# Optimization experiments

Measured on AMD Instinct MI355X. Metric: run time of the kernel, lower is better.

Reference implementation:

```python
import jax, jax.numpy as jnp
import numpy as np

B, S, E = 4, 4096, 512

def setup_inputs() -> dict:
    key = jax.random.key(0)
    ks = jax.random.split(key, 9)
    scale = 1.0 / np.sqrt(E)  # keep linear weights at realistic init scale
    return {
        "query": jax.random.normal(ks[0], (B, S, E), jnp.float32),
        "key":   jax.random.normal(ks[1], (B, S, E), jnp.float32),
        "value": jax.random.normal(ks[2], (B, S, E), jnp.float32),
        "Wq": jax.random.normal(ks[3], (E, E), jnp.float32) * scale,
        "bq": jax.random.normal(ks[4], (E,), jnp.float32) * scale,
        "Wk": jax.random.normal(ks[5], (E, E), jnp.float32) * scale,
        "bk": jax.random.normal(ks[6], (E,), jnp.float32) * scale,
        "Wv": jax.random.normal(ks[7], (E, E), jnp.float32) * scale,
        "bv": jax.random.normal(ks[8], (E,), jnp.float32) * scale,
    }

def reference(query, key, value, Wq, bq, Wk, bk, Wv, bv):
    # torch Linear: x @ W^T + b
    q = jnp.einsum('bse,oe->bso', query, Wq) + bq
    k = jnp.einsum('bse,oe->bso', key,   Wk) + bk
    v = jnp.einsum('bse,oe->bso', value, Wv) + bv
    # NOTE: module applies NO 1/sqrt(d) scaling (faithful to source)
    scores = jnp.einsum('bqd,bkd->bqk', q, k)          # [B,S,S] materialized
    attn = jax.nn.softmax(scores, axis=-1)
    # dropout is identity in eval / for deterministic reference
    return jnp.einsum('bqk,bkd->bqd', attn, v)         # [B,S,E]
```

## Files before the change

kernel.cpp:

```cpp
#include <hip/hip_runtime.h>

typedef __attribute__((ext_vector_type(8))) _Float16 f16x8;
typedef __attribute__((ext_vector_type(4))) _Float16 f16x4;
typedef __attribute__((ext_vector_type(4))) float f32x4;

#define NB 4
#define NS 4096
#define NE 512

__device__ __forceinline__ f16x8 cvt2(float4 a, float4 b) {
    f16x8 r;
    r[0] = (_Float16)a.x; r[1] = (_Float16)a.y; r[2] = (_Float16)a.z; r[3] = (_Float16)a.w;
    r[4] = (_Float16)b.x; r[5] = (_Float16)b.y; r[6] = (_Float16)b.z; r[7] = (_Float16)b.w;
    return r;
}
__device__ __forceinline__ void gload_lds16(const void* g, void* l) {
    __builtin_amdgcn_global_load_lds(
        (const __attribute__((address_space(1))) void*)g,
        (__attribute__((address_space(3))) void*)l, 16, 0, 0);
}

__global__ __launch_bounds__(256) void proj_kernel(
    const float* __restrict__ Xq, const float* __restrict__ Xk,
    const float* __restrict__ Xv,
    const float* __restrict__ Wq, const float* __restrict__ Wk,
    const float* __restrict__ Wv,
    const float* __restrict__ bq, const float* __restrict__ bk,
    const float* __restrict__ bv,
    _Float16* __restrict__ oq, _Float16* __restrict__ ok,
    _Float16* __restrict__ ovt, int b0)
{
    __shared__ __align__(16) _Float16 As[128 * 32];
    __shared__ __align__(16) _Float16 Bs[128 * 32];
    const int t = threadIdx.x;
    const int w = t >> 6, ln = t & 63;
    const int which = blockIdx.y;
    const float* X    = (which == 0) ? Xq : ((which == 1) ? Xk : Xv);
    const float* W    = (which == 0) ? Wq : ((which == 1) ? Wk : Wv);
    const float* bias = (which == 0) ? bq : ((which == 1) ? bk : bv);

    const int m0 = (blockIdx.x >> 2) * 128;
    const int n0 = (blockIdx.x & 3) * 128;

    const int srow  = t >> 1;
    const int shalf = (t & 1) * 16;
    const float* gA = X + ((size_t)b0 * NS + m0 + srow) * NE + shalf;
    const float* gB = W + (size_t)(n0 + srow) * NE + shalf;
    _Float16* lA = &As[srow * 32 + shalf];
    _Float16* lB = &Bs[srow * 32 + shalf];

    f32x4 acc[4][4] = {};
    const int wm = (w >> 1) * 64, wn = (w & 1) * 64;
    const int lcol = ln & 15, lq = ln >> 4;

    for (int k0 = 0; k0 < NE; k0 += 32) {
        float4 xa0 = *(const float4*)(gA + k0);
        float4 xa1 = *(const float4*)(gA + k0 + 4);
        float4 xa2 = *(const float4*)(gA + k0 + 8);
        float4 xa3 = *(const float4*)(gA + k0 + 12);
        float4 xb0 = *(const float4*)(gB + k0);
        float4 xb1 = *(const float4*)(gB + k0 + 4);
        float4 xb2 = *(const float4*)(gB + k0 + 8);
        float4 xb3 = *(const float4*)(gB + k0 + 12);
        __syncthreads();
        *(f16x8*)lA       = cvt2(xa0, xa1);
        *(f16x8*)(lA + 8) = cvt2(xa2, xa3);
        *(f16x8*)lB       = cvt2(xb0, xb1);
        *(f16x8*)(lB + 8) = cvt2(xb2, xb3);
        __syncthreads();
        f16x8 a[4], b[4];
#pragma unroll
        for (int i = 0; i < 4; i++)
            a[i] = *(const f16x8*)&As[(wm + i * 16 + lcol) * 32 + lq * 8];
#pragma unroll
        for (int j = 0; j < 4; j++)
            b[j] = *(const f16x8*)&Bs[(wn + j * 16 + lcol) * 32 + lq * 8];
#pragma unroll
        for (int i = 0; i < 4; i++)
#pragma unroll
            for (int j = 0; j < 4; j++)
                acc[i][j] = __builtin_amdgcn_mfma_f32_16x16x32_f16(a[i], b[j], acc[i][j], 0, 0, 0);
    }

    if (which == 0) {
#pragma unroll
        for (int j = 0; j < 4; j++) {
            const int col = n0 + wn + j * 16 + lcol;
            const float bb = bias[col];
#pragma unroll
            for (int i = 0; i < 4; i++) {
                const int rbase = m0 + wm + i * 16 + lq * 4;
#pragma unroll
                for (int r = 0; r < 4; r++)
                    oq[(size_t)(rbase + r) * NE + col] = (_Float16)(acc[i][j][r] + bb);
            }
        }
    } else if (which == 1) {
#pragma unroll
        for (int j = 0; j < 4; j++) {
            const int col = n0 + wn + j * 16 + lcol;
            const int cch = col >> 3, clo = col & 7;
            const float bb = bias[col];
#pragma unroll
            for (int i = 0; i < 4; i++) {
                const int rbase = m0 + wm + i * 16 + lq * 4;
#pragma unroll
                for (int r = 0; r < 4; r++) {
                    const int s = rbase + r;
                    ok[(size_t)s * NE + ((cch ^ (s & 7)) << 3) + clo] =
                        (_Float16)(acc[i][j][r] + bb);
                }
            }
        }
    } else {
#pragma unroll
        for (int j = 0; j < 4; j++) {
            const int d = n0 + wn + j * 16 + lcol;
            const float bb = bias[d];
#pragma unroll
            for (int i = 0; i < 4; i++) {
                const int rbase = m0 + wm + i * 16 + lq * 4;
                const int bat = rbase >> 12;
                const int sl  = rbase & 4095;
                const int kc  = sl >> 6;
                const int slot = ((sl >> 3) & 7) ^ (d & 7);
                f16x4 pk;
#pragma unroll
                for (int r = 0; r < 4; r++) pk[r] = (_Float16)(acc[i][j][r] + bb);
                *(f16x4*)&ovt[(((size_t)bat * 64 + kc) * NE + d) * 64 + slot * 8 + (sl & 7)] = pk;
            }
        }
    }
}

__global__ __launch_bounds__(512, 2) void attn_kernel(
    const _Float16* __restrict__ q, const _Float16* __restrict__ ksw,
    const _Float16* __restrict__ vsw, float* __restrict__ out, int b0)
{
    __shared__ __align__(16) _Float16 Kb[64 * 512];
    __shared__ __align__(16) _Float16 Vb[512 * 64];
    __shared__ __align__(16) _Float16 Pb[8][16 * 72];

    const int t = threadIdx.x, w = t >> 6, ln = t & 63;
    const int lcol = ln & 15, lq = ln >> 4;
    const int rt = w & 3, g = w >> 2;
    const int xm = lcol & 7;

    int qx, rel;
    if (gridDim.y == 4) {
        const int id = blockIdx.x + (blockIdx.y << 6);
        const int xcd = id & 7, slot = id >> 3;
        rel = xcd >> 1;
        qx  = ((xcd & 1) << 5) + slot;
    } else { qx = blockIdx.x; rel = blockIdx.y; }
    const int babs = b0 + rel;
    const int q0 = qx * 64;

    const _Float16* qp = q + ((size_t)rel * NS + q0 + rt * 16 + lcol) * NE + lq * 8;
    f16x8 qf[16];
#pragma unroll
    for (int ks = 0; ks < 16; ks++) qf[ks] = *(const f16x8*)(qp + ks * 32);

    const _Float16* kbase = ksw + (size_t)rel * NS * NE;
    const _Float16* vbase = vsw + (size_t)rel * NS * NE;

    f32x4 oacc[16] = {};
    float m_st[4] = {-1e30f, -1e30f, -1e30f, -1e30f};
    float l_st[4] = {0.f, 0.f, 0.f, 0.f};

    auto stageK = [&](int kc) {
        const _Float16* src = kbase + (size_t)kc * 64 * NE;
#pragma unroll
        for (int i = 0; i < 8; i++) {
            const int blk = i * 8 + w;
            gload_lds16(src + (size_t)blk * 512 + ln * 8, (_Float16*)Kb + blk * 512);
        }
    };
    auto stageV = [&](int kc) {
        const _Float16* src = vbase + (size_t)kc * NE * 64;
#pragma unroll
        for (int i = 0; i < 8; i++) {
            const int blk = i * 8 + w;
            gload_lds16(src + (size_t)blk * 512 + ln * 8, (_Float16*)Vb + blk * 512);
        }
    };

    stageK(0);
    stageV(0);

    for (int kc = 0; kc < 64; kc++) {
        asm volatile("s_waitcnt vmcnt(8)" ::: "memory");
        __builtin_amdgcn_s_barrier();
        asm volatile("" ::: "memory");

        f32x4 s0 = {}, s1 = {}, s2 = {}, s3 = {};
        __builtin_amdgcn_s_setprio(1);
#pragma unroll
        for (int ks = 0; ks < 16; ks++) {
            const int ch = ((ks * 4 + lq) ^ xm) * 8;
            f16x8 k0 = *(const f16x8*)&Kb[(lcol)      * 512 + ch];
            f16x8 k1 = *(const f16x8*)&Kb[(16 + lcol) * 512 + ch];
            f16x8 k2 = *(const f16x8*)&Kb[(32 + lcol) * 512 + ch];
            f16x8 k3 = *(const f16x8*)&Kb[(48 + lcol) * 512 + ch];
            s0 = __builtin_amdgcn_mfma_f32_16x16x32_f16(qf[ks], k0, s0, 0, 0, 0);
            s1 = __builtin_amdgcn_mfma_f32_16x16x32_f16(qf[ks], k1, s1, 0, 0, 0);
            s2 = __builtin_amdgcn_mfma_f32_16x16x32_f16(qf[ks], k2, s2, 0, 0, 0);
            s3 = __builtin_amdgcn_mfma_f32_16x16x32_f16(qf[ks], k3, s3, 0, 0, 0);
        }
        __builtin_amdgcn_s_setprio(0);

        asm volatile("" ::: "memory");
        __builtin_amdgcn_s_barrier();
        asm volatile("" ::: "memory");
        if (kc + 1 < 64) stageK(kc + 1);

        float alpha[4];
        float p0[4], p1[4], p2[4], p3[4];
#pragma unroll
        for (int r = 0; r < 4; r++) {
            float mx = fmaxf(fmaxf(s0[r], s1[r]), fmaxf(s2[r], s3[r]));
#pragma unroll
            for (int msk = 8; msk; msk >>= 1) mx = fmaxf(mx, __shfl_xor(mx, msk, 64));
            const float mn = fmaxf(m_st[r], mx);
            alpha[r] = __expf(m_st[r] - mn);
            p0[r] = __expf(s0[r] - mn);
            p1[r] = __expf(s1[r] - mn);
            p2[r] = __expf(s2[r] - mn);
            p3[r] = __expf(s3[r] - mn);
            float ls = (p0[r] + p1[r]) + (p2[r] + p3[r]);
#pragma unroll
            for (int msk = 8; msk; msk >>= 1) ls += __shfl_xor(ls, msk, 64);
            l_st[r] = l_st[r] * alpha[r] + ls;
            m_st[r] = mn;
            const int row = lq * 4 + r;
            Pb[w][row * 72 +      lcol] = (_Float16)p0[r];
            Pb[w][row * 72 + 16 + lcol] = (_Float16)p1[r];
            Pb[w][row * 72 + 32 + lcol] = (_Float16)p2[r];
            Pb[w][row * 72 + 48 + lcol] = (_Float16)p3[r];
        }
        const bool allone = (alpha[0] == 1.f) & (alpha[1] == 1.f) &
                            (alpha[2] == 1.f) & (alpha[3] == 1.f);
        if (!__all(allone)) {
#pragma unroll
            for (int et = 0; et < 16; et++) {
                oacc[et][0] *= alpha[0]; oacc[et][1] *= alpha[1];
                oacc[et][2] *= alpha[2]; oacc[et][3] *= alpha[3];
            }
        }
        f16x8 pa0 = *(const f16x8*)&Pb[w][lcol * 72 +      lq * 8];
        f16x8 pa1 = *(const f16x8*)&Pb[w][lcol * 72 + 32 + lq * 8];

        if (kc + 1 < 64) { asm volatile("s_waitcnt vmcnt(8)" ::: "memory"); }
        else             { asm volatile("s_waitcnt vmcnt(0)" ::: "memory"); }
        __builtin_amdgcn_s_barrier();
        asm volatile("" ::: "memory");

        __builtin_amdgcn_s_setprio(1);
#pragma unroll
        for (int et = 0; et < 16; et++) {
            const int e = g * 256 + et * 16 + lcol;
            f16x8 v0 = *(const f16x8*)&Vb[e * 64 + ((lq ^ xm) * 8)];
            f16x8 v1 = *(const f16x8*)&Vb[e * 64 + (((4 + lq) ^ xm) * 8)];
            oacc[et] = __builtin_amdgcn_mfma_f32_16x16x32_f16(pa0, v0, oacc[et], 0, 0, 0);
            oacc[et] = __builtin_amdgcn_mfma_f32_16x16x32_f16(pa1, v1, oacc[et], 0, 0, 0);
        }
        __builtin_amdgcn_s_setprio(0);

        if (kc + 1 < 64) {
            asm volatile("" ::: "memory");
            __builtin_amdgcn_s_barrier();
            asm volatile("" ::: "memory");
            stageV(kc + 1);
        }
    }

#pragma unroll
    for (int r = 0; r < 4; r++) {
        const float inv = 1.0f / l_st[r];
        const size_t ob = ((size_t)babs * NS + q0 + rt * 16 + lq * 4 + r) * NE + g * 256 + lcol;
#pragma unroll
        for (int et = 0; et < 16; et++)
            out[ob + et * 16] = oacc[et][r] * inv;
    }
}

extern "C" void kernel_launch(void* const* d_in, const int* in_sizes, int n_in,
                              void* d_out, int out_size, void* d_ws, size_t ws_size,
                              hipStream_t stream) {
    const float* query = (const float*)d_in[0];
    const float* key_  = (const float*)d_in[1];
    const float* value = (const float*)d_in[2];
    const float* Wq    = (const float*)d_in[3];
    const float* bq    = (const float*)d_in[4];
    const float* Wk    = (const float*)d_in[5];
    const float* bk    = (const float*)d_in[6];
    const float* Wv    = (const float*)d_in[7];
    const float* bv    = (const float*)d_in[8];

    const size_t per_batch = (size_t)3 * NS * NE * 2;
    int nb_chunk = (int)(ws_size / per_batch);
    if (nb_chunk > NB) nb_chunk = NB;
    if (nb_chunk < 1)  nb_chunk = 1;

    _Float16* qh  = (_Float16*)d_ws;
    _Float16* kh  = qh + (size_t)nb_chunk * NS * NE;
    _Float16* vth = kh + (size_t)nb_chunk * NS * NE;

    for (int b0 = 0; b0 < NB; b0 += nb_chunk) {
        int nb = NB - b0 < nb_chunk ? NB - b0 : nb_chunk;
        proj_kernel<<<dim3(nb * 128, 3, 1), 256, 0, stream>>>(
            query, key_, value, Wq, Wk, Wv, bq, bk, bv, qh, kh, vth, b0);
        attn_kernel<<<dim3(NS / 64, nb, 1), 512, 0, stream>>>(
            qh, kh, vth, (float*)d_out, b0);
    }
}
```

Before: 529.3 us.

## Split QK^T key columns across wave groups and merge softmax stats via LDS

Before, both wave groups computed the full 64-column QK^T score tile, each doing the same work. Now each group computes only its 32 key columns and keeps a local max and sum. The partial stats are exchanged through LDS so the online softmax can be merged, and the P fragments are rescaled in f16 before the PV MFMAs. Row reductions now use DPP row-rotate instead of shuffles. This halves the redundant score MFMAs and K LDS reads, but adds an LDS exchange, extra exps and f16 rescaling of P, which may cost some precision.

Measured after the change: 452.6 us. 14.5% less time.

```diff
diff --git a/kernel.cpp b/kernel.cpp
--- a/kernel.cpp
+++ b/kernel.cpp
@@ -18,6 +18,27 @@
     __builtin_amdgcn_global_load_lds(
         (const __attribute__((address_space(1))) void*)g,
         (__attribute__((address_space(3))) void*)l, 16, 0, 0);
+}
+
+template <int CTRL>
+__device__ __forceinline__ float dpp_ror(float x) {
+    int r = __builtin_amdgcn_update_dpp(
+        0, __builtin_bit_cast(int, x), CTRL, 0xF, 0xF, true);
+    return __builtin_bit_cast(float, r);
+}
+__device__ __forceinline__ float rmax16(float x) {
+    x = fmaxf(x, dpp_ror<0x128>(x));
+    x = fmaxf(x, dpp_ror<0x124>(x));
+    x = fmaxf(x, dpp_ror<0x122>(x));
+    x = fmaxf(x, dpp_ror<0x121>(x));
+    return x;
+}
+__device__ __forceinline__ float rsum16(float x) {
+    x += dpp_ror<0x128>(x);
+    x += dpp_ror<0x124>(x);
+    x += dpp_ror<0x122>(x);
+    x += dpp_ror<0x121>(x);
+    return x;
 }
 
 __global__ __launch_bounds__(256) void proj_kernel(
@@ -139,7 +160,9 @@
 {
     __shared__ __align__(16) _Float16 Kb[64 * 512];
     __shared__ __align__(16) _Float16 Vb[512 * 64];
-    __shared__ __align__(16) _Float16 Pb[8][16 * 72];
+    __shared__ __align__(16) _Float16 Pb[64 * 72];
+    __shared__ float mpart[2][64];
+    __shared__ float lpart[2][64];
 
     const int t = threadIdx.x, w = t >> 6, ln = t & 63;
     const int lcol = ln & 15, lq = ln >> 4;
@@ -164,27 +187,28 @@
     const _Float16* kbase = ksw + (size_t)rel * NS * NE;
     const _Float16* vbase = vsw + (size_t)rel * NS * NE;
 
+    auto stageK = [&](int kc) {
+        const _Float16* src = kbase + (size_t)kc * 64 * NE;
+#pragma unroll
+        for (int i = 0; i < 8; i++) {
+            const int blk = i * 8 + w;
+            gload_lds16(src + (size_t)blk * 512 + ln * 8, (_Float16*)Kb + blk * 512);
+        }
+    };
+    auto stageV = [&](int kc) {
+        const _Float16* src = vbase + (size_t)kc * NE * 64;
+#pragma unroll
+        for (int i = 0; i < 8; i++) {
+            const int blk = i * 8 + w;
+            gload_lds16(src + (size_t)blk * 512 + ln * 8, (_Float16*)Vb + blk * 512);
+        }
+    };
+
     f32x4 oacc[16] = {};
     float m_st[4] = {-1e30f, -1e30f, -1e30f, -1e30f};
     float l_st[4] = {0.f, 0.f, 0.f, 0.f};
 
-    auto stageK = [&](int kc) {
-        const _Float16* src = kbase + (size_t)kc * 64 * NE;
-#pragma unroll
-        for (int i = 0; i < 8; i++) {
-            const int blk = i * 8 + w;
-            gload_lds16(src + (size_t)blk * 512 + ln * 8, (_Float16*)Kb + blk * 512);
-        }
-    };
-    auto stageV = [&](int kc) {
-        const _Float16* src = vbase + (size_t)kc * NE * 64;
-#pragma unroll
-        for (int i = 0; i < 8; i++) {
-            const int blk = i * 8 + w;
-            gload_lds16(src + (size_t)blk * 512 + ln * 8, (_Float16*)Vb + blk * 512);
-        }
-    };
-
+    asm volatile("" ::: "memory");
     stageK(0);
     stageV(0);
 
@@ -193,50 +217,53 @@
         __builtin_amdgcn_s_barrier();
         asm volatile("" ::: "memory");
 
-        f32x4 s0 = {}, s1 = {}, s2 = {}, s3 = {};
+        f32x4 s0 = {}, s1 = {};
         __builtin_amdgcn_s_setprio(1);
 #pragma unroll
         for (int ks = 0; ks < 16; ks++) {
             const int ch = ((ks * 4 + lq) ^ xm) * 8;
-            f16x8 k0 = *(const f16x8*)&Kb[(lcol)      * 512 + ch];
-            f16x8 k1 = *(const f16x8*)&Kb[(16 + lcol) * 512 + ch];
-            f16x8 k2 = *(const f16x8*)&Kb[(32 + lcol) * 512 + ch];
-            f16x8 k3 = *(const f16x8*)&Kb[(48 + lcol) * 512 + ch];
-            s0 = __builtin_amdgcn_mfma_f32_16x16x32_f16(qf[ks], k0, s0, 0, 0, 0);
-            s1 = __builtin_amdgcn_mfma_f32_16x16x32_f16(qf[ks], k1, s1, 0, 0, 0);
-            s2 = __builtin_amdgcn_mfma_f32_16x16x32_f16(qf[ks], k2, s2, 0, 0, 0);
-            s3 = __builtin_amdgcn_mfma_f32_16x16x32_f16(qf[ks], k3, s3, 0, 0, 0);
+            f16x8 kb0 = *(const f16x8*)&Kb[(g * 32 + lcol) * 512 + ch];
+            f16x8 kb1 = *(const f16x8*)&Kb[(g * 32 + 16 + lcol) * 512 + ch];
+            s0 = __builtin_amdgcn_mfma_f32_16x16x32_f16(qf[ks], kb0, s0, 0, 0, 0);
+            s1 = __builtin_amdgcn_mfma_f32_16x16x32_f16(qf[ks], kb1, s1, 0, 0, 0);
         }
         __builtin_amdgcn_s_setprio(0);
 
         asm volatile("" ::: "memory");
         __builtin_amdgcn_s_barrier();
         asm volatile("" ::: "memory");
-        if (kc + 1 < 64) stageK(kc + 1);
+        if (kc < 63) stageK(kc + 1);
+
+        float Mg[4];
+#pragma unroll
+        for (int r = 0; r < 4; r++) {
+            float mx = rmax16(fmaxf(s0[r], s1[r]));
+            Mg[r] = fmaxf(m_st[r], mx);
+            const float p0 = __expf(s0[r] - Mg[r]);
+            const float p1 = __expf(s1[r] - Mg[r]);
+            const int row = rt * 16 + lq * 4 + r;
+            Pb[row * 72 + g * 32 + lcol]      = (_Float16)p0;
+            Pb[row * 72 + g * 32 + 16 + lcol] = (_Float16)p1;
+            const float ls = rsum16(p0 + p1);
+            if (lcol == 0) { mpart[g][row] = Mg[r]; lpart[g][row] = ls; }
+        }
+
+        if (kc < 63) { asm volatile("s_waitcnt vmcnt(8) lgkmcnt(0)" ::: "memory"); }
+        else         { asm volatile("s_waitcnt vmcnt(0) lgkmcnt(0)" ::: "memory"); }
+        __builtin_amdgcn_s_barrier();
+        asm volatile("" ::: "memory");
 
         float alpha[4];
-        float p0[4], p1[4], p2[4], p3[4];
 #pragma unroll
         for (int r = 0; r < 4; r++) {
-            float mx = fmaxf(fmaxf(s0[r], s1[r]), fmaxf(s2[r], s3[r]));
-#pragma unroll
-            for (int msk = 8; msk; msk >>= 1) mx = fmaxf(mx, __shfl_xor(mx, msk, 64));
-            const float mn = fmaxf(m_st[r], mx);
+            const int row = rt * 16 + lq * 4 + r;
+            const float M0 = mpart[0][row], M1 = mpart[1][row];
+            const float mn = fmaxf(M0, M1);
             alpha[r] = __expf(m_st[r] - mn);
-            p0[r] = __expf(s0[r] - mn);
-            p1[r] = __expf(s1[r] - mn);
-            p2[r] = __expf(s2[r] - mn);
-            p3[r] = __expf(s3[r] - mn);
-            float ls = (p0[r] + p1[r]) + (p2[r] + p3[r]);
-#pragma unroll
-            for (int msk = 8; msk; msk >>= 1) ls += __shfl_xor(ls, msk, 64);
-            l_st[r] = l_st[r] * alpha[r] + ls;
+            l_st[r] = l_st[r] * alpha[r]
+                    + __expf(M0 - mn) * lpart[0][row]
+                    + __expf(M1 - mn) * lpart[1][row];
             m_st[r] = mn;
-            const int row = lq * 4 + r;
-            Pb[w][row * 72 +      lcol] = (_Float16)p0[r];
-            Pb[w][row * 72 + 16 + lcol] = (_Float16)p1[r];
-            Pb[w][row * 72 + 32 + lcol] = (_Float16)p2[r];
-            Pb[w][row * 72 + 48 + lcol] = (_Float16)p3[r];
         }
         const bool allone = (alpha[0] == 1.f) & (alpha[1] == 1.f) &
                             (alpha[2] == 1.f) & (alpha[3] == 1.f);
@@ -247,13 +274,16 @@
                 oacc[et][2] *= alpha[2]; oacc[et][3] *= alpha[3];
             }
         }
-        f16x8 pa0 = *(const f16x8*)&Pb[w][lcol * 72 +      lq * 8];
-        f16x8 pa1 = *(const f16x8*)&Pb[w][lcol * 72 + 32 + lq * 8];
-
-        if (kc + 1 < 64) { asm volatile("s_waitcnt vmcnt(8)" ::: "memory"); }
-        else             { asm volatile("s_waitcnt vmcnt(0)" ::: "memory"); }
-        __builtin_amdgcn_s_barrier();
-        asm volatile("" ::: "memory");
+
+        const int frow = rt * 16 + lcol;
+        const float F0 = mpart[0][frow], F1 = mpart[1][frow];
+        const float fm = fmaxf(F0, F1);
+        const _Float16 c0 = (_Float16)__expf(F0 - fm);
+        const _Float16 c1 = (_Float16)__expf(F1 - fm);
+        f16x8 pa0 = *(const f16x8*)&Pb[frow * 72 + lq * 8];
+        f16x8 pa1 = *(const f16x8*)&Pb[frow * 72 + 32 + lq * 8];
+#pragma unroll
+        for (int j = 0; j < 8; j++) { pa0[j] *= c0; pa1[j] *= c1; }
 
         __builtin_amdgcn_s_setprio(1);
 #pragma unroll
@@ -266,12 +296,10 @@
         }
         __builtin_amdgcn_s_setprio(0);
 
-        if (kc + 1 < 64) {
-            asm volatile("" ::: "memory");
-            __builtin_amdgcn_s_barrier();
-            asm volatile("" ::: "memory");
-            stageV(kc + 1);
-        }
+        asm volatile("" ::: "memory");
+        __builtin_amdgcn_s_barrier();
+        asm volatile("" ::: "memory");
+        if (kc < 63) stageV(kc + 1);
     }
 
 #pragma unroll
```
